# Performance work log

Measured on AMD Instinct MI355X. Metric: run time of the kernel, lower is better.

## Reference

```python
import jax, jax.numpy as jnp
import numpy as np

D_MODEL = 256
D_EDGE = 64
EPS = 1e-05
INPUT_FEATS = 2 * D_MODEL + D_EDGE + 1  # 577


def _linear_params(key, fan_in, fan_out):
    k1, k2 = jax.random.split(key)
    lim = 1.0 / np.sqrt(fan_in)
    W = jax.random.uniform(k1, (fan_in, fan_out), minval=-lim, maxval=lim, dtype=jnp.float32)
    b = jax.random.uniform(k2, (fan_out,), minval=-lim, maxval=lim, dtype=jnp.float32)
    return W, b


def setup_inputs() -> dict:
    key = jax.random.key(0)
    ks = jax.random.split(key, 16)
    B, N = 8, 128
    inp = {
        "coords": jax.random.normal(ks[0], (B, N, 3), dtype=jnp.float32),
        "inv_feats": jax.random.normal(ks[1], (B, N, D_MODEL), dtype=jnp.float32),
        "adj_matrix": jnp.ones((B, N, N), dtype=jnp.float32),
        "atom_mask": jnp.ones((B, N), dtype=jnp.float32),
        "edge_feats": jax.random.normal(ks[2], (B, N, N, D_EDGE), dtype=jnp.float32),
    }
    inp["W_e1"], inp["b_e1"] = _linear_params(ks[3], INPUT_FEATS, D_MODEL)
    inp["W_e2"], inp["b_e2"] = _linear_params(ks[4], D_MODEL, D_MODEL)
    inp["W_att"], inp["b_att"] = _linear_params(ks[5], D_MODEL, 1)
    inp["W_h1"], inp["b_h1"] = _linear_params(ks[6], 2 * D_MODEL, D_MODEL)
    inp["W_h2"], inp["b_h2"] = _linear_params(ks[7], D_MODEL, D_MODEL)
    inp["W_x1"], inp["b_x1"] = _linear_params(ks[8], INPUT_FEATS, D_MODEL)
    inp["W_x2"], inp["b_x2"] = _linear_params(ks[9], D_MODEL, D_MODEL)
    inp["W_x3"], inp["b_x3"] = _linear_params(ks[10], D_MODEL, 1)
    return inp


def _pair_linear(W, b, node_feats, ef):
    # Linear over concat([node_i, node_j, ef]) without materializing the concat.
    # W: [2*d_model + d_edge + 1, out]
    d = D_MODEL
    hi = node_feats @ W[:d]          # [B,N,out]
    hj = node_feats @ W[d:2 * d]     # [B,N,out]
    he = ef @ W[2 * d:]              # [B,N,N,out]
    return hi[:, :, None, :] + hj[:, None, :, :] + he + b


def _egnn_forward(coords, inv_feats, adj_matrix, atom_mask, edge_feats,
                  W_e1, b_e1, W_e2, b_e2, W_att, b_att,
                  W_h1, b_h1, W_h2, b_h2, W_x1, b_x1, W_x2, b_x2, W_x3, b_x3):
    mask = atom_mask[..., None]                       # [B,N,1]
    diff = coords[:, :, None, :] - coords[:, None, :, :]   # [B,N,N,3]
    sq = jnp.sum(diff * diff, axis=-1, keepdims=True)      # [B,N,N,1]
    ef = jnp.concatenate([edge_feats, sq], axis=-1)        # [B,N,N,d_edge+1]
    adj = adj_matrix[..., None]                             # [B,N,N,1]

    # phi_e: Linear-SiLU-Linear-SiLU on pair features
    msg = jax.nn.silu(_pair_linear(W_e1, b_e1, inv_feats, ef))
    msg = jax.nn.silu(msg @ W_e2 + b_e2)                    # [B,N,N,d]

    att = jax.nn.sigmoid(msg @ W_att + b_att)               # [B,N,N,1]
    node_msg = jnp.sum(msg * att * adj, axis=2)             # [B,N,d]

    h = jnp.concatenate([inv_feats, node_msg], axis=-1)
    h = jax.nn.silu(h @ W_h1 + b_h1) @ W_h2 + b_h2          # [B,N,d]

    # phi_x: Linear-SiLU-Linear-SiLU-Linear -> scalar per edge
    ex = jax.nn.silu(_pair_linear(W_x1, b_x1, inv_feats, ef))
    ex = jax.nn.silu(ex @ W_x2 + b_x2)
    edge_attn = ex @ W_x3 + b_x3                             # [B,N,N,1]

    normalisers = jnp.sqrt(sq[..., 0] + EPS) + 1.0           # [B,N,N]
    weighted = diff * edge_attn / normalisers[..., None] * adj
    coord_updates = jnp.sum(weighted, axis=2)                # [B,N,3]
    num_nodes = jnp.sum(mask, axis=1) + 1.0                  # [B,1]
    coord_updates = coord_updates / num_nodes[:, :, None]

    out_coords = (coords + coord_updates) * mask
    out_feats = h * mask
    return out_coords, out_feats


def reference(coords, inv_feats, adj_matrix, atom_mask, edge_feats,
              W_e1, b_e1, W_e2, b_e2, W_att, b_att,
              W_h1, b_h1, W_h2, b_h2, W_x1, b_x1, W_x2, b_x2, W_x3, b_x3):
    return _egnn_forward(coords, inv_feats, adj_matrix, atom_mask, edge_feats,
                         W_e1, b_e1, W_e2, b_e2, W_att, b_att,
                         W_h1, b_h1, W_h2, b_h2, W_x1, b_x1, W_x2, b_x2, W_x3, b_x3)
```

## Files before the change

### kernel.cpp

```cpp
#include <hip/hip_runtime.h>

typedef __attribute__((ext_vector_type(8))) __bf16 bf16x8;
typedef __attribute__((ext_vector_type(4))) __bf16 bf16x4;
typedef __attribute__((ext_vector_type(4))) float f32x4;

#define SCHED0 __builtin_amdgcn_sched_barrier(0)

__device__ __forceinline__ float fast_sig(float x) {
  return __builtin_amdgcn_rcpf(1.0f + __expf(-x));
}
__device__ __forceinline__ float siluf(float x) { return x * fast_sig(x); }
__device__ __forceinline__ __bf16 tobf(float x) { return (__bf16)x; }

__global__ __launch_bounds__(256) void k_prep(
    const float* __restrict__ We1, const float* __restrict__ Wx1,
    const float* __restrict__ We2, const float* __restrict__ Wx2,
    const float* __restrict__ Wh1, const float* __restrict__ Wh2,
    const float* __restrict__ invf,
    __bf16* __restrict__ wt_e, __bf16* __restrict__ wt_x,
    __bf16* __restrict__ w2e, __bf16* __restrict__ w2x,
    __bf16* __restrict__ wh1t, __bf16* __restrict__ wh2t,
    __bf16* __restrict__ invb,
    float* __restrict__ nmsg, float* __restrict__ cupd)
{
  int idx = blockIdx.x * 256 + threadIdx.x;
  if (idx < 147456) {
    int kk = idx / 576, f = idx - kk * 576;
    wt_e[idx] = tobf(We1[f * 256 + kk]);
    wt_x[idx] = tobf(Wx1[f * 256 + kk]);
  }
  if (idx < 65536) {
    int c = idx >> 8, k = idx & 255;
    w2e[idx] = tobf(We2[k * 256 + c]);
    w2x[idx] = tobf(Wx2[k * 256 + c]);
    wh2t[idx] = tobf(Wh2[k * 256 + c]);
    f32x4 z = {0.f, 0.f, 0.f, 0.f};
    *(f32x4*)(nmsg + idx * 4) = z;
  }
  if (idx < 131072) {
    int c = idx >> 9, k = idx & 511;
    wh1t[idx] = tobf(Wh1[k * 256 + c]);
  }
  if (idx < 3072) cupd[idx] = 0.f;
  invb[idx] = tobf(invf[idx]);
}

template<int NKS>
__device__ __forceinline__ void node_gemm64(
    const __bf16* __restrict__ B, int ldb, int boff,
    const __bf16* __restrict__ A, int lda, int aoff,
    int row0, int tid, f32x4 acc[4][4])
{
  const int lane = tid & 63, wc = tid >> 6, lr = lane & 15, lg = lane >> 4;
  #pragma unroll
  for (int ks = 0; ks < NKS; ks++) {
    bf16x8 bB[4], aA[4];
    #pragma unroll
    for (int m = 0; m < 4; m++)
      bB[m] = *(const bf16x8*)(B + (size_t)(row0 + m * 16 + lr) * ldb + boff + ks * 32 + lg * 8);
    #pragma unroll
    for (int n = 0; n < 4; n++)
      aA[n] = *(const bf16x8*)(A + (size_t)(wc * 64 + n * 16 + lr) * lda + aoff + ks * 32 + lg * 8);
    #pragma unroll
    for (int m = 0; m < 4; m++)
      #pragma unroll
      for (int n = 0; n < 4; n++)
        acc[m][n] = __builtin_amdgcn_mfma_f32_16x16x32_bf16(aA[n], bB[m], acc[m][n], 0, 0, 0);
  }
}

__global__ __launch_bounds__(256) void k_nproj(
    const __bf16* __restrict__ invb,
    const __bf16* __restrict__ wt_e, const __bf16* __restrict__ wt_x,
    const float* __restrict__ be1, const float* __restrict__ bx1,
    float* __restrict__ hie, float* __restrict__ hix,
    __bf16* __restrict__ hje, __bf16* __restrict__ hjx)
{
  const int tid = threadIdx.x;
  const int row0 = blockIdx.x * 64;
  const int mat = blockIdx.y;
  const __bf16* A = (mat < 2) ? wt_e : wt_x;
  const int aoff = (mat & 1) ? 256 : 0;

  f32x4 acc[4][4];
  #pragma unroll
  for (int m = 0; m < 4; m++)
    #pragma unroll
    for (int n = 0; n < 4; n++) { f32x4 z = {0.f,0.f,0.f,0.f}; acc[m][n] = z; }
  node_gemm64<8>(invb, 256, 0, A, 576, aoff, row0, tid, acc);

  const int lane = tid & 63, wc = tid >> 6, lr = lane & 15, lg = lane >> 4;
  if ((mat & 1) == 0) {
    const float* bias = (mat == 0) ? be1 : bx1;
    float* out = (mat == 0) ? hie : hix;
    #pragma unroll
    for (int m = 0; m < 4; m++) {
      int node = row0 + m * 16 + lr;
      #pragma unroll
      for (int n = 0; n < 4; n++) {
        int c0 = wc * 64 + n * 16 + lg * 4;
        f32x4 v = acc[m][n] + *(const f32x4*)(bias + c0);
        *(f32x4*)(out + (size_t)node * 256 + c0) = v;
      }
    }
  } else {
    __bf16* out = (mat == 1) ? hje : hjx;
    #pragma unroll
    for (int m = 0; m < 4; m++) {
      int node = row0 + m * 16 + lr;
      #pragma unroll
      for (int n = 0; n < 4; n++) {
        int c0 = wc * 64 + n * 16 + lg * 4;
        bf16x4 pk;
        #pragma unroll
        for (int r = 0; r < 4; r++) pk[r] = tobf(acc[m][n][r]);
        *(bf16x4*)(out + (size_t)node * 256 + c0) = pk;
      }
    }
  }
}

__global__ __launch_bounds__(256) void k_h1(
    const __bf16* __restrict__ invb, const float* __restrict__ nmsg,
    const __bf16* __restrict__ wh1t,
    const float* __restrict__ bh1, __bf16* __restrict__ h1b)
{
  const int tid = threadIdx.x;
  const int row0 = blockIdx.x * 64;
  const int c0 = blockIdx.y * 64;
  const int lane = tid & 63, w = tid >> 6, lr = lane & 15, lg = lane >> 4;
  const int node = row0 + w * 16 + lr;

  f32x4 acc[4];
  #pragma unroll
  for (int n = 0; n < 4; n++) { f32x4 z = {0.f,0.f,0.f,0.f}; acc[n] = z; }

  #pragma unroll
  for (int ks = 0; ks < 16; ks++) {
    bf16x8 bB;
    if (ks < 8) {
      bB = *(const bf16x8*)(invb + (size_t)node * 256 + ks * 32 + lg * 8);
    } else {
      const float* pp = nmsg + (size_t)node * 256 + (ks - 8) * 32 + lg * 8;
      f32x4 lo = *(const f32x4*)pp;
      f32x4 hi = *(const f32x4*)(pp + 4);
      bf16x8 t;
      t[0]=tobf(lo[0]); t[1]=tobf(lo[1]); t[2]=tobf(lo[2]); t[3]=tobf(lo[3]);
      t[4]=tobf(hi[0]); t[5]=tobf(hi[1]); t[6]=tobf(hi[2]); t[7]=tobf(hi[3]);
      bB = t;
    }
    #pragma unroll
    for (int n = 0; n < 4; n++) {
      bf16x8 aA = *(const bf16x8*)(wh1t + (size_t)(c0 + n * 16 + lr) * 512 + ks * 32 + lg * 8);
      acc[n] = __builtin_amdgcn_mfma_f32_16x16x32_bf16(aA, bB, acc[n], 0, 0, 0);
    }
  }

  #pragma unroll
  for (int n = 0; n < 4; n++) {
    int cc = c0 + n * 16 + lg * 4;
    f32x4 b4 = *(const f32x4*)(bh1 + cc);
    bf16x4 pk;
    #pragma unroll
    for (int r = 0; r < 4; r++) pk[r] = tobf(siluf(acc[n][r] + b4[r]));
    *(bf16x4*)(h1b + (size_t)node * 256 + cc) = pk;
  }
}

__global__ __launch_bounds__(256) void k_h2(
    const __bf16* __restrict__ h1b, const __bf16* __restrict__ wh2t,
    const float* __restrict__ bh2, const float* __restrict__ amask,
    const float* __restrict__ coords, const float* __restrict__ cupd,
    float* __restrict__ out_feats, float* __restrict__ out_coords)
{
  __shared__ float sM[2];
  const int tid = threadIdx.x;
  const int row0 = blockIdx.x * 64;
  const int c0 = blockIdx.y * 64;
  const int b = row0 >> 7;
  const int lane = tid & 63, w = tid >> 6, lr = lane & 15, lg = lane >> 4;
  const int node = row0 + w * 16 + lr;

  f32x4 acc[4];
  #pragma unroll
  for (int n = 0; n < 4; n++) { f32x4 z = {0.f,0.f,0.f,0.f}; acc[n] = z; }

  #pragma unroll
  for (int ks = 0; ks < 8; ks++) {
    bf16x8 bB = *(const bf16x8*)(h1b + (size_t)node * 256 + ks * 32 + lg * 8);
    #pragma unroll
    for (int n = 0; n < 4; n++) {
      bf16x8 aA = *(const bf16x8*)(wh2t + (size_t)(c0 + n * 16 + lr) * 256 + ks * 32 + lg * 8);
      acc[n] = __builtin_amdgcn_mfma_f32_16x16x32_bf16(aA, bB, acc[n], 0, 0, 0);
    }
  }

  float msk = amask[node];
  #pragma unroll
  for (int n = 0; n < 4; n++) {
    int cc = c0 + n * 16 + lg * 4;
    f32x4 b4 = *(const f32x4*)(bh2 + cc);
    f32x4 v = (acc[n] + b4) * msk;
    *(f32x4*)(out_feats + (size_t)node * 256 + cc) = v;
  }

  if (blockIdx.y == 0) {
    if (tid < 128) {
      float v = amask[b * 128 + tid];
      #pragma unroll
      for (int off = 1; off < 64; off <<= 1) v += __shfl_xor(v, off);
      if ((tid & 63) == 0) sM[tid >> 6] = v;
    }
    __syncthreads();
    const float sNum = sM[0] + sM[1];
    if (tid < 192) {
      int nl = tid / 3, d = tid - nl * 3;
      int nd = row0 + nl;
      float upd = cupd[nd * 3 + d] / (sNum + 1.0f);
      out_coords[nd * 3 + d] = (coords[nd * 3 + d] + upd) * amask[nd];
    }
  }
}

__global__ __launch_bounds__(512, 2) void k_edge(
    const float* __restrict__ coords, const float* __restrict__ adjm,
    const float* __restrict__ ef,
    const float* __restrict__ We1, const float* __restrict__ Wx1,
    const float* __restrict__ batt,
    const float* __restrict__ be2, const float* __restrict__ bx2,
    const float* __restrict__ bx3,
    const float* __restrict__ Watt, const float* __restrict__ Wx3,
    const float* __restrict__ hie, const float* __restrict__ hix,
    const __bf16* __restrict__ hje, const __bf16* __restrict__ hjx,
    const __bf16* __restrict__ wt_e, const __bf16* __restrict__ wt_x,
    const __bf16* __restrict__ w2e, const __bf16* __restrict__ w2x,
    float* __restrict__ nmsg, float* __restrict__ cupd)
{
  __shared__ __align__(16) char sSb[64 * 512];
  __shared__ __align__(16) __bf16 sE[64 * 72];
  __shared__ float sqv[64], sAdj[2][64], sRed[2][64];

  const int tid = threadIdx.x;
  const int p = blockIdx.x & 1;
  const int widx = blockIdx.x >> 1;
  const int lane = tid & 63;
  const int wv = tid >> 6;
  const int lr = lane & 15, lg = lane >> 4;
  const int cg = wv * 32;

  const __bf16* wt = p ? wt_x : wt_e;
  const __bf16* w2 = p ? w2x : w2e;
  const float* hi_mat = p ? hix : hie;
  const __bf16* hj_mat = p ? hjx : hje;
  const float* slast_g = (p ? Wx1 : We1) + 576 * 256;
  const float b0 = p ? bx3[0] : batt[0];

  f32x4 bb[2], vv[2], sl[2];
  #pragma unroll
  for (int n = 0; n < 2; n++) {
    bb[n] = *(const f32x4*)((p ? bx2 : be2) + cg + n * 16 + lg * 4);
    vv[n] = *(const f32x4*)((p ? Wx3 : Watt) + cg + n * 16 + lg * 4);
    sl[n] = *(const f32x4*)(slast_g + cg + n * 16 + lg * 4);
  }

  bf16x8 aW1[2][2], aW2[8][2];
  #pragma unroll
  for (int ks = 0; ks < 2; ks++)
    #pragma unroll
    for (int n = 0; n < 2; n++)
      aW1[ks][n] = *(const bf16x8*)(wt + (size_t)(cg + n * 16 + lr) * 576 + 512 + ks * 32 + lg * 8);
  #pragma unroll
  for (int ks = 0; ks < 8; ks++)
    #pragma unroll
    for (int n = 0; n < 2; n++)
      aW2[ks][n] = *(const bf16x8*)(w2 + (size_t)(cg + n * 16 + lr) * 256 + ks * 32 + lg * 8);

  for (int t = 0; t < 8; ++t) {
    const int h = widx * 8 + t;
    const int bi = h >> 1;
    const int b = bi >> 7;
    const int jg0 = b * 128 + (h & 1) * 64;

    if (tid < 64) {
      sRed[t & 1][tid] = 0.f;
      int jg = jg0 + tid;
      float dx = coords[bi * 3 + 0] - coords[jg * 3 + 0];
      float dy = coords[bi * 3 + 1] - coords[jg * 3 + 1];
      float dz = coords[bi * 3 + 2] - coords[jg * 3 + 2];
      sqv[tid] = dx * dx + dy * dy + dz * dz;
    } else if (tid < 128) {
      sAdj[t & 1][tid - 64] = adjm[(size_t)bi * 128 + (h & 1) * 64 + (tid - 64)];
    }
    {
      const float* efb = ef + ((size_t)bi * 128 + (h & 1) * 64) * 64;
      int row = tid >> 3, col = (tid & 7) * 8;
      const float* er = efb + row * 64 + col;
      f32x4 x = *(const f32x4*)er;
      f32x4 y = *(const f32x4*)(er + 4);
      bf16x8 e8;
      e8[0] = tobf(x[0]); e8[1] = tobf(x[1]); e8[2] = tobf(x[2]); e8[3] = tobf(x[3]);
      e8[4] = tobf(y[0]); e8[5] = tobf(y[1]); e8[6] = tobf(y[2]); e8[7] = tobf(y[3]);
      *(bf16x8*)(sE + row * 72 + col) = e8;
    }
    SCHED0;
    asm volatile("s_waitcnt lgkmcnt(0)" ::: "memory");
    __builtin_amdgcn_s_barrier();
    SCHED0;

    f32x4 hi4[2];
    bf16x4 hj4[4][2];
    #pragma unroll
    for (int n = 0; n < 2; n++)
      hi4[n] = *(const f32x4*)(hi_mat + (size_t)bi * 256 + cg + n * 16 + lg * 4);
    #pragma unroll
    for (int m = 0; m < 4; m++)
      #pragma unroll
      for (int n = 0; n < 2; n++)
        hj4[m][n] = *(const bf16x4*)(hj_mat + (size_t)(jg0 + m * 16 + lr) * 256 + cg + n * 16 + lg * 4);

    f32x4 acc[4][2];
    #pragma unroll
    for (int m = 0; m < 4; m++)
      #pragma unroll
      for (int n = 0; n < 2; n++) { f32x4 z = {0.f,0.f,0.f,0.f}; acc[m][n] = z; }

    #pragma unroll
    for (int ks = 0; ks < 2; ks++) {
      bf16x8 bE[4];
      #pragma unroll
      for (int m = 0; m < 4; m++)
        bE[m] = *(const bf16x8*)(sE + (m * 16 + lr) * 72 + ks * 32 + lg * 8);
      __builtin_amdgcn_s_setprio(1);
      #pragma unroll
      for (int m = 0; m < 4; m++)
        #pragma unroll
        for (int n = 0; n < 2; n++)
          acc[m][n] = __builtin_amdgcn_mfma_f32_16x16x32_bf16(aW1[ks][n], bE[m], acc[m][n], 0, 0, 0);
      __builtin_amdgcn_s_setprio(0);
    }

    #pragma unroll
    for (int m = 0; m < 4; m++) {
      const int jl = m * 16 + lr;
      const float sq = sqv[jl];
      #pragma unroll
      for (int n = 0; n < 2; n++) {
        const int kk0 = cg + n * 16 + lg * 4;
        bf16x4 pk;
        #pragma unroll
        for (int r = 0; r < 4; r++) {
          float v = acc[m][n][r] + hi4[n][r] + (float)hj4[m][n][r] + sq * sl[n][r];
          pk[r] = tobf(siluf(v));
        }
        int off = (jl * 512 + kk0 * 2) ^ ((jl & 7) << 4);
        *(bf16x4*)(sSb + off) = pk;
        f32x4 z = {0.f, 0.f, 0.f, 0.f};
        acc[m][n] = z;
      }
    }
    SCHED0;
    asm volatile("s_waitcnt lgkmcnt(0)" ::: "memory");
    __builtin_amdgcn_s_barrier();
    SCHED0;

    #pragma unroll
    for (int ks = 0; ks < 8; ks++) {
      bf16x8 bS[4];
      #pragma unroll
      for (int m = 0; m < 4; m++) {
        const int jl = m * 16 + lr;
        int off = (jl * 512 + (ks * 32 + lg * 8) * 2) ^ ((jl & 7) << 4);
        bS[m] = *(const bf16x8*)(sSb + off);
      }
      __builtin_amdgcn_s_setprio(1);
      #pragma unroll
      for (int m = 0; m < 4; m++)
        #pragma unroll
        for (int n = 0; n < 2; n++)
          acc[m][n] = __builtin_amdgcn_mfma_f32_16x16x32_bf16(aW2[ks][n], bS[m], acc[m][n], 0, 0, 0);
      __builtin_amdgcn_s_setprio(0);
    }

    float pr[4] = {0.f, 0.f, 0.f, 0.f};
    #pragma unroll
    for (int n = 0; n < 2; n++) {
      #pragma unroll
      for (int m = 0; m < 4; m++)
        #pragma unroll
        for (int r = 0; r < 4; r++) {
          float s = siluf(acc[m][n][r] + bb[n][r]);
          acc[m][n][r] = s;
          pr[m] += s * vv[n][r];
        }
    }
    #pragma unroll
    for (int m = 0; m < 4; m++) {
      pr[m] += __shfl_xor(pr[m], 16);
      pr[m] += __shfl_xor(pr[m], 32);
    }
    if (lane < 16) {
      #pragma unroll
      for (int m = 0; m < 4; m++)
        atomicAdd(&sRed[t & 1][m * 16 + lr], pr[m]);
    }
    SCHED0;
    asm volatile("s_waitcnt lgkmcnt(0)" ::: "memory");
    __builtin_amdgcn_s_barrier();
    SCHED0;

    if (p == 0) {
      float aw[4];
      #pragma unroll
      for (int m = 0; m < 4; m++)
        aw[m] = fast_sig(sRed[t & 1][m * 16 + lr] + b0) * sAdj[t & 1][m * 16 + lr];
      f32x4 q[2];
      #pragma unroll
      for (int n = 0; n < 2; n++) { f32x4 z = {0.f,0.f,0.f,0.f}; q[n] = z; }
      #pragma unroll
      for (int m = 0; m < 4; m++)
        #pragma unroll
        for (int n = 0; n < 2; n++)
          q[n] += acc[m][n] * aw[m];
      #pragma unroll
      for (int off = 1; off < 16; off <<= 1)
        #pragma unroll
        for (int n = 0; n < 2; n++)
          #pragma unroll
          for (int r = 0; r < 4; r++)
            q[n][r] += __shfl_xor(q[n][r], off);
      if (lr == 0) {
        #pragma unroll
        for (int n = 0; n < 2; n++)
          #pragma unroll
          for (int r = 0; r < 4; r++)
            atomicAdd(&nmsg[(size_t)bi * 256 + cg + n * 16 + lg * 4 + r], q[n][r]);
      }
    } else {
      if (tid < 64) {
        int jl = tid;
        int jgl = jg0 + jl;
        float ea = sRed[t & 1][jl] + b0;
        float wgt = ea * __builtin_amdgcn_rcpf(sqrtf(sqv[jl] + 1e-5f) + 1.0f) * sAdj[t & 1][jl];
        float wx = wgt * (coords[bi * 3 + 0] - coords[jgl * 3 + 0]);
        float wy = wgt * (coords[bi * 3 + 1] - coords[jgl * 3 + 1]);
        float wz = wgt * (coords[bi * 3 + 2] - coords[jgl * 3 + 2]);
        #pragma unroll
        for (int off = 1; off < 64; off <<= 1) {
          wx += __shfl_xor(wx, off);
          wy += __shfl_xor(wy, off);
          wz += __shfl_xor(wz, off);
        }
        if (tid == 0) {
          atomicAdd(&cupd[bi * 3 + 0], wx);
          atomicAdd(&cupd[bi * 3 + 1], wy);
          atomicAdd(&cupd[bi * 3 + 2], wz);
        }
      }
    }
  }
}

extern "C" void kernel_launch(void* const* d_in, const int* in_sizes, int n_in,
                              void* d_out, int out_size, void* d_ws, size_t ws_size,
                              hipStream_t stream)
{
  const float* coords = (const float*)d_in[0];
  const float* invf  = (const float*)d_in[1];
  const float* adjm  = (const float*)d_in[2];
  const float* amask = (const float*)d_in[3];
  const float* ef    = (const float*)d_in[4];
  const float* We1   = (const float*)d_in[5];
  const float* be1   = (const float*)d_in[6];
  const float* We2   = (const float*)d_in[7];
  const float* be2   = (const float*)d_in[8];
  const float* Watt  = (const float*)d_in[9];
  const float* batt  = (const float*)d_in[10];
  const float* Wh1   = (const float*)d_in[11];
  const float* bh1   = (const float*)d_in[12];
  const float* Wh2   = (const float*)d_in[13];
  const float* bh2   = (const float*)d_in[14];
  const float* Wx1   = (const float*)d_in[15];
  const float* bx1   = (const float*)d_in[16];
  const float* Wx2   = (const float*)d_in[17];
  const float* bx2   = (const float*)d_in[18];
  const float* Wx3   = (const float*)d_in[19];
  const float* bx3   = (const float*)d_in[20];

  char* ws = (char*)d_ws;
  const size_t MB = 1u << 20;
  float*  hie  = (float*)(ws + 0 * MB);
  float*  hix  = (float*)(ws + 1 * MB);
  __bf16* hje  = (__bf16*)(ws + 2 * MB);
  __bf16* hjx  = (__bf16*)(ws + 2 * MB + 524288);
  __bf16* invb = (__bf16*)(ws + 3 * MB);
  __bf16* h1b  = (__bf16*)(ws + 3 * MB + 524288);
  size_t woff = 4 * MB;
  __bf16* wt_e = (__bf16*)(ws + woff);
  __bf16* wt_x = (__bf16*)(ws + woff + 294912);
  __bf16* w2e  = (__bf16*)(ws + woff + 2 * 294912);
  __bf16* w2x  = (__bf16*)(ws + woff + 2 * 294912 + 131072);
  __bf16* wh1t = (__bf16*)(ws + woff + 2 * 294912 + 2 * 131072);
  __bf16* wh2t = (__bf16*)(ws + woff + 2 * 294912 + 2 * 131072 + 262144);
  float*  nmsg = (float*)(ws + 5 * MB + 524288);
  float*  cupd = (float*)(ws + 6 * MB + 524288);

  float* out_coords = (float*)d_out;
  float* out_feats  = out_coords + 8 * 128 * 3;

  hipLaunchKernelGGL(k_prep, dim3(1024), dim3(256), 0, stream,
                     We1, Wx1, We2, Wx2, Wh1, Wh2, invf,
                     wt_e, wt_x, w2e, w2x, wh1t, wh2t, invb, nmsg, cupd);
  hipLaunchKernelGGL(k_nproj, dim3(16, 4), dim3(256), 0, stream,
                     invb, wt_e, wt_x, be1, bx1, hie, hix, hje, hjx);
  hipLaunchKernelGGL(k_edge, dim3(512), dim3(512), 0, stream,
                     coords, adjm, ef, We1, Wx1, batt, be2, bx2, bx3, Watt, Wx3,
                     hie, hix, hje, hjx, wt_e, wt_x, w2e, w2x, nmsg, cupd);
  hipLaunchKernelGGL(k_h1, dim3(16, 4), dim3(256), 0, stream,
                     invb, nmsg, wh1t, bh1, h1b);
  hipLaunchKernelGGL(k_h2, dim3(16, 4), dim3(256), 0, stream,
                     h1b, wh2t, bh2, amask, coords, cupd, out_feats, out_coords);
}
```

Baseline: 151.5 us.

## Double-buffer edge tile staging and prefetch next tile during second GEMM

Splits the edge-feature, squared-distance and adjacency shared buffers into two slots. The next tile's global loads are issued before the second MFMA GEMM and written to shared memory after it, which removes one barrier per iteration and hides global load latency. It also remaps block index so the e-path and x-path blocks are grouped in runs of eight instead of interleaved. In exchange it uses more LDS and more registers for the prefetched values, which may hurt occupancy at two blocks per CU.

```diff
diff --git a/kernel.cpp b/kernel.cpp
--- a/kernel.cpp
+++ b/kernel.cpp
@@ -3,8 +3,6 @@
 typedef __attribute__((ext_vector_type(8))) __bf16 bf16x8;
 typedef __attribute__((ext_vector_type(4))) __bf16 bf16x4;
 typedef __attribute__((ext_vector_type(4))) float f32x4;
-
-#define SCHED0 __builtin_amdgcn_sched_barrier(0)
 
 __device__ __forceinline__ float fast_sig(float x) {
   return __builtin_amdgcn_rcpf(1.0f + __expf(-x));
@@ -237,22 +235,20 @@
     float* __restrict__ nmsg, float* __restrict__ cupd)
 {
   __shared__ __align__(16) char sSb[64 * 512];
-  __shared__ __align__(16) __bf16 sE[64 * 72];
-  __shared__ float sqv[64], sAdj[2][64], sRed[2][64];
+  __shared__ __align__(16) __bf16 sE[2][64 * 72];
+  __shared__ float sqv[2][64], sAdj[2][64], sRed[2][64];
 
   const int tid = threadIdx.x;
-  const int p = blockIdx.x & 1;
-  const int widx = blockIdx.x >> 1;
+  const int d = blockIdx.x;
+  const int p = (d >> 3) & 1;
+  const int widx = (d >> 4) * 8 + (d & 7);
   const int lane = tid & 63;
   const int wv = tid >> 6;
   const int lr = lane & 15, lg = lane >> 4;
   const int cg = wv * 32;
 
-  const __bf16* wt = p ? wt_x : wt_e;
-  const __bf16* w2 = p ? w2x : w2e;
   const float* hi_mat = p ? hix : hie;
   const __bf16* hj_mat = p ? hjx : hje;
-  const float* slast_g = (p ? Wx1 : We1) + 576 * 256;
   const float b0 = p ? bx3[0] : batt[0];
 
   f32x4 bb[2], vv[2], sl[2];
@@ -260,9 +256,11 @@
   for (int n = 0; n < 2; n++) {
     bb[n] = *(const f32x4*)((p ? bx2 : be2) + cg + n * 16 + lg * 4);
     vv[n] = *(const f32x4*)((p ? Wx3 : Watt) + cg + n * 16 + lg * 4);
-    sl[n] = *(const f32x4*)(slast_g + cg + n * 16 + lg * 4);
-  }
-
+    sl[n] = *(const f32x4*)(((p ? Wx1 : We1) + 576 * 256) + cg + n * 16 + lg * 4);
+  }
+
+  const __bf16* wt = p ? wt_x : wt_e;
+  const __bf16* w2 = p ? w2x : w2e;
   bf16x8 aW1[2][2], aW2[8][2];
   #pragma unroll
   for (int ks = 0; ks < 2; ks++)
@@ -274,38 +272,40 @@
     #pragma unroll
     for (int n = 0; n < 2; n++)
       aW2[ks][n] = *(const bf16x8*)(w2 + (size_t)(cg + n * 16 + lr) * 256 + ks * 32 + lg * 8);
+
+  const int erow = tid >> 3;
+  const int ecol = (tid & 7) * 8;
+
+  {
+    const int h = widx * 8;
+    const int bi0 = h >> 1;
+    const int jg00 = (bi0 >> 7) * 128;
+    if (tid < 64) {
+      sRed[0][tid] = 0.f;
+      int jg = jg00 + tid;
+      float dx = coords[bi0 * 3 + 0] - coords[jg * 3 + 0];
+      float dy = coords[bi0 * 3 + 1] - coords[jg * 3 + 1];
+      float dz = coords[bi0 * 3 + 2] - coords[jg * 3 + 2];
+      sqv[0][tid] = dx * dx + dy * dy + dz * dz;
+    } else if (tid < 128) {
+      sAdj[0][tid - 64] = adjm[(size_t)bi0 * 128 + (tid - 64)];
+    }
+    const float* er = ef + (size_t)bi0 * 8192 + erow * 64 + ecol;
+    f32x4 x = *(const f32x4*)er;
+    f32x4 y = *(const f32x4*)(er + 4);
+    bf16x8 e8;
+    e8[0]=tobf(x[0]); e8[1]=tobf(x[1]); e8[2]=tobf(x[2]); e8[3]=tobf(x[3]);
+    e8[4]=tobf(y[0]); e8[5]=tobf(y[1]); e8[6]=tobf(y[2]); e8[7]=tobf(y[3]);
+    *(bf16x8*)(&sE[0][0] + erow * 72 + ecol) = e8;
+  }
+  __syncthreads();
 
   for (int t = 0; t < 8; ++t) {
     const int h = widx * 8 + t;
     const int bi = h >> 1;
-    const int b = bi >> 7;
-    const int jg0 = b * 128 + (h & 1) * 64;
-
-    if (tid < 64) {
-      sRed[t & 1][tid] = 0.f;
-      int jg = jg0 + tid;
-      float dx = coords[bi * 3 + 0] - coords[jg * 3 + 0];
-      float dy = coords[bi * 3 + 1] - coords[jg * 3 + 1];
-      float dz = coords[bi * 3 + 2] - coords[jg * 3 + 2];
-      sqv[tid] = dx * dx + dy * dy + dz * dz;
-    } else if (tid < 128) {
-      sAdj[t & 1][tid - 64] = adjm[(size_t)bi * 128 + (h & 1) * 64 + (tid - 64)];
-    }
-    {
-      const float* efb = ef + ((size_t)bi * 128 + (h & 1) * 64) * 64;
-      int row = tid >> 3, col = (tid & 7) * 8;
-      const float* er = efb + row * 64 + col;
-      f32x4 x = *(const f32x4*)er;
-      f32x4 y = *(const f32x4*)(er + 4);
-      bf16x8 e8;
-      e8[0] = tobf(x[0]); e8[1] = tobf(x[1]); e8[2] = tobf(x[2]); e8[3] = tobf(x[3]);
-      e8[4] = tobf(y[0]); e8[5] = tobf(y[1]); e8[6] = tobf(y[2]); e8[7] = tobf(y[3]);
-      *(bf16x8*)(sE + row * 72 + col) = e8;
-    }
-    SCHED0;
-    asm volatile("s_waitcnt lgkmcnt(0)" ::: "memory");
-    __builtin_amdgcn_s_barrier();
-    SCHED0;
+    const int jg0 = (bi >> 7) * 128 + (h & 1) * 64;
+    const int cur = t & 1;
+    const __bf16* sEc = &sE[cur][0];
 
     f32x4 hi4[2];
     bf16x4 hj4[4][2];
@@ -329,7 +329,7 @@
       bf16x8 bE[4];
       #pragma unroll
       for (int m = 0; m < 4; m++)
-        bE[m] = *(const bf16x8*)(sE + (m * 16 + lr) * 72 + ks * 32 + lg * 8);
+        bE[m] = *(const bf16x8*)(sEc + (m * 16 + lr) * 72 + ks * 32 + lg * 8);
       __builtin_amdgcn_s_setprio(1);
       #pragma unroll
       for (int m = 0; m < 4; m++)
@@ -342,7 +342,7 @@
     #pragma unroll
     for (int m = 0; m < 4; m++) {
       const int jl = m * 16 + lr;
-      const float sq = sqv[jl];
+      const float sq = sqv[cur][jl];
       #pragma unroll
       for (int n = 0; n < 2; n++) {
         const int kk0 = cg + n * 16 + lg * 4;
@@ -358,10 +358,26 @@
         acc[m][n] = z;
       }
     }
-    SCHED0;
-    asm volatile("s_waitcnt lgkmcnt(0)" ::: "memory");
-    __builtin_amdgcn_s_barrier();
-    SCHED0;
+    __syncthreads();
+
+    f32x4 ex, ey;
+    float nx = 0.f, ny = 0.f, nz = 0.f, njx = 0.f, njy = 0.f, njz = 0.f, nadj = 0.f;
+    int bi_n = 0, jg0_n = 0;
+    if (t < 7) {
+      const int hn = h + 1;
+      bi_n = hn >> 1;
+      jg0_n = (bi_n >> 7) * 128 + (hn & 1) * 64;
+      const float* er = ef + ((size_t)bi_n * 128 + (hn & 1) * 64) * 64 + erow * 64 + ecol;
+      ex = *(const f32x4*)er;
+      ey = *(const f32x4*)(er + 4);
+      if (tid < 64) {
+        int jg = jg0_n + tid;
+        nx = coords[bi_n * 3 + 0]; ny = coords[bi_n * 3 + 1]; nz = coords[bi_n * 3 + 2];
+        njx = coords[jg * 3 + 0]; njy = coords[jg * 3 + 1]; njz = coords[jg * 3 + 2];
+      } else if (tid < 128) {
+        nadj = adjm[(size_t)bi_n * 128 + ((hn & 1) * 64) + (tid - 64)];
+      }
+    }
 
     #pragma unroll
     for (int ks = 0; ks < 8; ks++) {
@@ -401,18 +417,30 @@
     if (lane < 16) {
       #pragma unroll
       for (int m = 0; m < 4; m++)
-        atomicAdd(&sRed[t & 1][m * 16 + lr], pr[m]);
-    }
-    SCHED0;
-    asm volatile("s_waitcnt lgkmcnt(0)" ::: "memory");
-    __builtin_amdgcn_s_barrier();
-    SCHED0;
+        atomicAdd(&sRed[cur][m * 16 + lr], pr[m]);
+    }
+
+    if (t < 7) {
+      const int nxt = cur ^ 1;
+      bf16x8 e8;
+      e8[0]=tobf(ex[0]); e8[1]=tobf(ex[1]); e8[2]=tobf(ex[2]); e8[3]=tobf(ex[3]);
+      e8[4]=tobf(ey[0]); e8[5]=tobf(ey[1]); e8[6]=tobf(ey[2]); e8[7]=tobf(ey[3]);
+      *(bf16x8*)(&sE[nxt][0] + erow * 72 + ecol) = e8;
+      if (tid < 64) {
+        sRed[nxt][tid] = 0.f;
+        float dx = nx - njx, dy = ny - njy, dz = nz - njz;
+        sqv[nxt][tid] = dx * dx + dy * dy + dz * dz;
+      } else if (tid < 128) {
+        sAdj[nxt][tid - 64] = nadj;
+      }
+    }
+    __syncthreads();
 
     if (p == 0) {
       float aw[4];
       #pragma unroll
       for (int m = 0; m < 4; m++)
-        aw[m] = fast_sig(sRed[t & 1][m * 16 + lr] + b0) * sAdj[t & 1][m * 16 + lr];
+        aw[m] = fast_sig(sRed[cur][m * 16 + lr] + b0) * sAdj[cur][m * 16 + lr];
       f32x4 q[2];
       #pragma unroll
       for (int n = 0; n < 2; n++) { f32x4 z = {0.f,0.f,0.f,0.f}; q[n] = z; }
@@ -439,8 +467,8 @@
       if (tid < 64) {
         int jl = tid;
         int jgl = jg0 + jl;
-        float ea = sRed[t & 1][jl] + b0;
-        float wgt = ea * __builtin_amdgcn_rcpf(sqrtf(sqv[jl] + 1e-5f) + 1.0f) * sAdj[t & 1][jl];
+        float ea = sRed[cur][jl] + b0;
+        float wgt = ea * __builtin_amdgcn_rcpf(sqrtf(sqv[cur][jl] + 1e-5f) + 1.0f) * sAdj[cur][jl];
         float wx = wgt * (coords[bi * 3 + 0] - coords[jgl * 3 + 0]);
         float wy = wgt * (coords[bi * 3 + 1] - coords[jgl * 3 + 1]);
         float wz = wgt * (coords[bi * 3 + 2] - coords[jgl * 3 + 2]);
```

After: 150.3 us, median of 2. Within noise of the previous version (-0.8%).
